# Performance work log

Hardware: AMD Instinct MI355X
Metric: run time of the kernel (lower is better)

The kernel has to match this reference:

```python
import jax, jax.numpy as jnp
import numpy as np

INPUT_DIMS = 3
K = 64          # num_bases_per_dim
DEG = 3         # cubic
MIN_VAL = -1.0
MAX_VAL = 1.0
SCALE = (K - DEG) / (MAX_VAL - MIN_VAL)
EPS = 1e-6
N_POINTS = 1_000_000


def setup_inputs() -> dict:
    key = jax.random.key(0)
    x = jax.random.uniform(key, (N_POINTS, INPUT_DIMS), jnp.float32,
                           minval=-1.0, maxval=1.0)
    return {"x": x}


def reference(x):
    N, D = x.shape
    # scale to knot space and clamp so idx+3 <= K-1
    xs = jnp.clip((x - MIN_VAL) * SCALE, 0.0, K - DEG - EPS)
    idx = jnp.floor(xs).astype(jnp.int32)          # [N, D]
    u = xs - idx.astype(xs.dtype)                  # local coord in [0,1)
    u2 = u * u
    u3 = u2 * u
    c0 = (1.0 - u) ** 3 / 6.0
    c1 = (3.0 * u3 - 6.0 * u2 + 4.0) / 6.0
    c2 = (-3.0 * u3 + 3.0 * u2 + 3.0 * u + 1.0) / 6.0
    c3 = u3 / 6.0
    coeffs = jnp.stack([c0, c1, c2, c3], axis=-1)  # [N, D, 4]
    idxs = idx[..., None] + jnp.arange(4, dtype=jnp.int32)  # [N, D, 4]
    # scatter 4 active coefficients into K bins per (point, dim)
    bn = jnp.arange(N)[:, None, None]
    dn = jnp.arange(D)[None, :, None]
    feat = jnp.zeros((N, D, K), dtype=x.dtype).at[bn, dn, idxs].set(coeffs)
    # include_input=True: per-dim layout [x_d, feat_d] then concat over dims
    out = jnp.concatenate([x[:, :, None], feat], axis=2).reshape(N, D * (1 + K))
    return out
```

## Files before the change

kernel.cpp:

```cpp
#include <hip/hip_runtime.h>


typedef float vfloat4 __attribute__((ext_vector_type(4)));

constexpr int   DIMS        = 3;
constexpr int   K           = 64;
constexpr int   ROW         = DIMS * (1 + K);
constexpr float SCALE       = 30.5f;
constexpr float CLAMP_MAX   = 61.0f - 1e-6f;
constexpr int   PTS_PER_BLK = 64;
constexpr int   PAIRS       = PTS_PER_BLK * DIMS;
constexpr int   FLT_PER_BLK = PTS_PER_BLK * ROW;
constexpr int   V4_PER_BLK  = FLT_PER_BLK / 4;

__global__ __launch_bounds__(256)
void bspline_kernel(const float* __restrict__ x, float* __restrict__ out,
                    int n_pairs_total) {
    __shared__ __align__(16) float params[(PAIRS + 1) * 8];
    const int t = threadIdx.x;

    if (t < PAIRS) {
        const int gp = blockIdx.x * PAIRS + t;
        float xv = 0.0f;
        if (gp < n_pairs_total) xv = x[gp];
        float xs = (xv + 1.0f) * SCALE;
        xs = fminf(fmaxf(xs, 0.0f), CLAMP_MAX);
        const int   idx = (int)xs;
        const float u   = xs - (float)idx;
        const float u2  = u * u;
        const float u3  = u2 * u;
        const float om  = 1.0f - u;
        float* rec = params + t * 8;
        rec[0] = xv;
        rec[1] = __int_as_float(idx);
        rec[2] = om * om * om * (1.0f / 6.0f);
        rec[3] = (3.0f * u3 - 6.0f * u2 + 4.0f) * (1.0f / 6.0f);
        rec[4] = (-3.0f * u3 + 3.0f * u2 + 3.0f * u + 1.0f) * (1.0f / 6.0f);
        rec[5] = u3 * (1.0f / 6.0f);
    }
    if (t == 255) {
        float* rec = params + PAIRS * 8;
#pragma unroll
        for (int i = 0; i < 8; ++i) rec[i] = 0.0f;
    }
    __syncthreads();

    const float4* p4 = reinterpret_cast<const float4*>(params);
    vfloat4* out4 = reinterpret_cast<vfloat4*>(out)
                  + (long long)blockIdx.x * V4_PER_BLK;

    for (int f = t; f < V4_PER_BLK; f += 256) {
        const int pos = f * 4;
        const int p   = pos / 65;
        const int j   = pos - p * 65;
        const int p2  = p + ((j >= 62) ? 1 : 0);

        const float4 a0 = p4[p * 2];
        const float4 a1 = p4[p * 2 + 1];
        const float4 b0 = p4[p2 * 2];
        const float4 b1 = p4[p2 * 2 + 1];
        const int ia = __float_as_int(a0.y);
        const int ib = __float_as_int(b0.y);

        vfloat4 comp;
#pragma unroll
        for (int c = 0; c < 4; ++c) {
            const int  o  = j + c;
            const bool cr = (o >= 65);
            const int  oo = cr ? (o - 65) : o;
            const float xv = cr ? b0.x : a0.x;
            const float k0 = cr ? b0.z : a0.z;
            const float k1 = cr ? b0.w : a0.w;
            const float k2 = cr ? b1.x : a1.x;
            const float k3 = cr ? b1.y : a1.y;
            const int  tt = oo - 1 - (cr ? ib : ia);
            float v = 0.0f;
            v = (tt == 0) ? k0 : v;
            v = (tt == 1) ? k1 : v;
            v = (tt == 2) ? k2 : v;
            v = (tt == 3) ? k3 : v;
            v = (oo == 0) ? xv : v;
            comp[c] = v;
        }
        __builtin_nontemporal_store(comp, &out4[f]);
    }
}

extern "C" void kernel_launch(void* const* d_in, const int* in_sizes, int n_in,
                              void* d_out, int out_size, void* d_ws, size_t ws_size,
                              hipStream_t stream) {
    const float* x  = (const float*)d_in[0];
    float* out      = (float*)d_out;
    const int n_pts = in_sizes[0] / DIMS;
    const int nblk  = (n_pts + PTS_PER_BLK - 1) / PTS_PER_BLK;
    bspline_kernel<<<dim3(nblk), dim3(256), 0, stream>>>(x, out, n_pts * DIMS);
}
```

Before: 766.7 us.

## Stage full output tile in shared memory instead of computing per-float4 selects

Each block now zero-fills a shared-memory tile holding its 64 rows of 195 floats, scatters each pair's x value and four coefficients into it, then copies the tile to global memory with batched float4 nontemporal stores. This removes the per-output divide-by-65 indexing and select chains of the previous version. In exchange the block uses about 50KB of LDS, which limits occupancy, and adds an extra barrier plus an LDS write and read of the whole tile. The scalar scatter writes with stride 65 may also hit bank conflicts.

```diff
diff --git a/kernel.cpp b/kernel.cpp
--- a/kernel.cpp
+++ b/kernel.cpp
@@ -12,12 +12,21 @@
 constexpr int   PAIRS       = PTS_PER_BLK * DIMS;
 constexpr int   FLT_PER_BLK = PTS_PER_BLK * ROW;
 constexpr int   V4_PER_BLK  = FLT_PER_BLK / 4;
+constexpr int   FULL_ITERS  = V4_PER_BLK / 256;
+constexpr int   TAIL        = V4_PER_BLK - FULL_ITERS * 256;
 
 __global__ __launch_bounds__(256)
 void bspline_kernel(const float* __restrict__ x, float* __restrict__ out,
                     int n_pairs_total) {
-    __shared__ __align__(16) float params[(PAIRS + 1) * 8];
+    __shared__ __align__(16) float tile[FLT_PER_BLK];
+    vfloat4* t4 = reinterpret_cast<vfloat4*>(tile);
     const int t = threadIdx.x;
+
+    const vfloat4 z = {0.0f, 0.0f, 0.0f, 0.0f};
+#pragma unroll
+    for (int i = 0; i < FULL_ITERS; ++i) t4[t + i * 256] = z;
+    if (t < TAIL) t4[FULL_ITERS * 256 + t] = z;
+    __syncthreads();
 
     if (t < PAIRS) {
         const int gp = blockIdx.x * PAIRS + t;
@@ -30,59 +39,26 @@
         const float u2  = u * u;
         const float u3  = u2 * u;
         const float om  = 1.0f - u;
-        float* rec = params + t * 8;
-        rec[0] = xv;
-        rec[1] = __int_as_float(idx);
-        rec[2] = om * om * om * (1.0f / 6.0f);
-        rec[3] = (3.0f * u3 - 6.0f * u2 + 4.0f) * (1.0f / 6.0f);
-        rec[4] = (-3.0f * u3 + 3.0f * u2 + 3.0f * u + 1.0f) * (1.0f / 6.0f);
-        rec[5] = u3 * (1.0f / 6.0f);
-    }
-    if (t == 255) {
-        float* rec = params + PAIRS * 8;
-#pragma unroll
-        for (int i = 0; i < 8; ++i) rec[i] = 0.0f;
+        float* base = tile + t * 65;
+        base[0]       = xv;
+        base[1 + idx] = om * om * om * (1.0f / 6.0f);
+        base[2 + idx] = (3.0f * u3 - 6.0f * u2 + 4.0f) * (1.0f / 6.0f);
+        base[3 + idx] = (-3.0f * u3 + 3.0f * u2 + 3.0f * u + 1.0f) * (1.0f / 6.0f);
+        base[4 + idx] = u3 * (1.0f / 6.0f);
     }
     __syncthreads();
 
-    const float4* p4 = reinterpret_cast<const float4*>(params);
     vfloat4* out4 = reinterpret_cast<vfloat4*>(out)
                   + (long long)blockIdx.x * V4_PER_BLK;
-
-    for (int f = t; f < V4_PER_BLK; f += 256) {
-        const int pos = f * 4;
-        const int p   = pos / 65;
-        const int j   = pos - p * 65;
-        const int p2  = p + ((j >= 62) ? 1 : 0);
-
-        const float4 a0 = p4[p * 2];
-        const float4 a1 = p4[p * 2 + 1];
-        const float4 b0 = p4[p2 * 2];
-        const float4 b1 = p4[p2 * 2 + 1];
-        const int ia = __float_as_int(a0.y);
-        const int ib = __float_as_int(b0.y);
-
-        vfloat4 comp;
+    vfloat4 v[FULL_ITERS];
 #pragma unroll
-        for (int c = 0; c < 4; ++c) {
-            const int  o  = j + c;
-            const bool cr = (o >= 65);
-            const int  oo = cr ? (o - 65) : o;
-            const float xv = cr ? b0.x : a0.x;
-            const float k0 = cr ? b0.z : a0.z;
-            const float k1 = cr ? b0.w : a0.w;
-            const float k2 = cr ? b1.x : a1.x;
-            const float k3 = cr ? b1.y : a1.y;
-            const int  tt = oo - 1 - (cr ? ib : ia);
-            float v = 0.0f;
-            v = (tt == 0) ? k0 : v;
-            v = (tt == 1) ? k1 : v;
-            v = (tt == 2) ? k2 : v;
-            v = (tt == 3) ? k3 : v;
-            v = (oo == 0) ? xv : v;
-            comp[c] = v;
-        }
-        __builtin_nontemporal_store(comp, &out4[f]);
+    for (int i = 0; i < FULL_ITERS; ++i) v[i] = t4[t + i * 256];
+#pragma unroll
+    for (int i = 0; i < FULL_ITERS; ++i)
+        __builtin_nontemporal_store(v[i], &out4[t + i * 256]);
+    if (t < TAIL) {
+        const vfloat4 vt = t4[FULL_ITERS * 256 + t];
+        __builtin_nontemporal_store(vt, &out4[FULL_ITERS * 256 + t]);
     }
 }
 
```

Measured after the change: 763.7 us. About the same (-0.4%).
